# Kernel tuning notes

Hardware: AMD Instinct MI355X
Metric: run time of the kernel (lower is better)

## Reference

```python
import jax, jax.numpy as jnp
import numpy as np

B, C, H, W = 2, 4, 32, 256   # batch, num_classes (class 0 = background), range-image H x W
N = H * W                    # candidate points per (batch, class)
RADIUS = 3.0
KM_ITERS = 1
COORD_SCALE = 60.0           # spread lidar x/y so radius-3 NMS is non-trivial


def setup_inputs() -> dict:
    key = jax.random.key(0)
    k1, k2 = jax.random.split(key)
    segmented_channels = jax.random.normal(k1, (B, C, H, W), dtype=jnp.float32)
    lidar = jax.random.normal(k2, (B, 2, H, W), dtype=jnp.float32) * COORD_SCALE
    return {"segmented_channels": segmented_channels, "lidar": lidar}


def _radius_nms(points, mask, radius):
    # Greedy radius NMS in index order: keep point i iff no earlier kept point
    # lies within `radius`. Masked-out points are never kept (keep init = mask).
    n = points.shape[0]
    idx = jnp.arange(n)
    r2 = radius * radius

    def step(keep, i):
        d2 = jnp.sum((points - points[i]) ** 2, axis=-1)       # [N]
        suppress = keep & (d2 < r2) & (idx > i) & keep[i]
        return keep & ~suppress, None

    keep, _ = jax.lax.scan(step, mask, idx)
    return keep


def _kmeans(points, mask, keep, iters):
    # Centers initialized at the NMS-kept points (same index space as points).
    # Each valid class point is assigned to nearest valid center; centers move
    # to the mean of their assigned points.
    n = points.shape[0]
    centers = points
    w = mask.astype(points.dtype)
    BIG = jnp.asarray(1e30, points.dtype)
    for _ in range(iters):
        d2 = jnp.sum((points[:, None, :] - centers[None, :, :]) ** 2, axis=-1)  # [N,N]
        d2 = jnp.where(keep[None, :], d2, BIG)
        assign = jnp.argmin(d2, axis=1)                         # [N]
        sums = jax.ops.segment_sum(points * w[:, None], assign, num_segments=n)
        cnt = jax.ops.segment_sum(w, assign, num_segments=n)
        upd = sums / jnp.maximum(cnt, 1.0)[:, None]
        centers = jnp.where((keep & (cnt > 0))[:, None], upd, centers)
    return centers * keep[:, None].astype(points.dtype)


def reference(segmented_channels, lidar):
    ind = jnp.argmax(segmented_channels, axis=1)                # [B,H,W] class id per cell
    pts = jnp.stack([lidar[:, 0], lidar[:, 1]], axis=-1).reshape(B, N, 2)
    # boolean class masks for foreground classes 1..C-1
    cls_mask = jnp.stack([ind == c for c in range(1, C)], axis=1).reshape(B, C - 1, N)
    pts_all = jnp.broadcast_to(pts[:, None], (B, C - 1, N, 2)).reshape(B * (C - 1), N, 2)
    mask_all = cls_mask.reshape(B * (C - 1), N)

    def per_bc(args):
        p, m = args
        keep = _radius_nms(p, m, RADIUS)
        centers = _kmeans(p, m, keep, KM_ITERS)
        return centers, keep

    centers, keep = jax.lax.map(per_bc, (pts_all, mask_all))
    # centers: padded [B, C-1, N, 2]; keep marks which rows are real detections
    return centers.reshape(B, C - 1, N, 2), keep.reshape(B, C - 1, N)
```

## Files before the change

kernel.cpp:

```cpp
#include <hip/hip_runtime.h>

#define NPTS 8192
#define BCLS 4
#define NP   6
#define R2   9.0f
#define RAD  3.0f
#define GRD  128
#define NCELL (GRD*GRD)
#define PCAP 2048
#define CAP  4096
#define KBLK 64
#define KTHR 256
#define NSL  8
#define WBLK (NP*NSL)
#define WTHR 256

#define ST_U 0u
#define ST_A 1u
#define ST_D 2u


__global__ __launch_bounds__(KTHR) void k_front(
    const float* __restrict__ seg, const float* __restrict__ lidar,
    float* __restrict__ xs, float* __restrict__ ys,
    unsigned int* __restrict__ ns, unsigned int* __restrict__ counts,
    float* __restrict__ ksum, float* __restrict__ out)
{
    const int tid = threadIdx.x, lane = tid & 63;
    const int idx = blockIdx.x * KTHR + tid;
    const int b = idx >> 13, n = idx & 8191;

    __shared__ float ex[KTHR], ey[KTHR];
    __shared__ unsigned short en[KTHR];
    __shared__ unsigned int cnt6[6], off6[6], pos6[6];

    if (tid < 6) cnt6[tid] = 0;
    __syncthreads();

    const float* segb = seg + (size_t)b * BCLS * NPTS + n;
    float bv = segb[0];
    int bc = 0;
    #pragma unroll
    for (int c = 1; c < BCLS; ++c) {
        float v = segb[(size_t)c * NPTS];
        if (v > bv) { bv = v; bc = c; }
    }
    const float x = lidar[(size_t)b * 2 * NPTS + n];
    const float y = lidar[(size_t)b * 2 * NPTS + NPTS + n];
    const int p = (bc > 0) ? (b * 3 + bc - 1) : -1;

    #pragma unroll
    for (int q = 0; q < 6; ++q) {
        unsigned long long bal = __ballot(p == q);
        if (lane == 0 && bal) atomicAdd(&cnt6[q], (unsigned int)__popcll(bal));
    }
    __syncthreads();
    if (tid == 0) {
        unsigned int a = 0;
        #pragma unroll
        for (int q = 0; q < 6; ++q) { off6[q] = a; pos6[q] = a; a += cnt6[q]; }
    }
    __syncthreads();
    #pragma unroll
    for (int q = 0; q < 6; ++q) {
        unsigned long long bal = __ballot(p == q);
        if (bal) {
            int ldr = __builtin_ctzll(bal);
            unsigned int wb = 0;
            if (lane == ldr) wb = atomicAdd(&pos6[q], (unsigned int)__popcll(bal));
            wb = __shfl(wb, ldr, 64);
            if (p == q) {
                unsigned int s = wb + (unsigned int)__popcll(bal & ((1ull << lane) - 1ull));
                ex[s] = x; ey[s] = y; en[s] = (unsigned short)n;
            }
        }
    }
    __syncthreads();
    {
        const unsigned int total = off6[5] + cnt6[5];
        const int gbase = blockIdx.x * KTHR;
        for (int k = tid; k < (int)total; k += KTHR) {
            xs[gbase + k] = ex[k];
            ys[gbase + k] = ey[k];
            ns[gbase + k] = (unsigned int)en[k];
        }
        if (tid < 6) counts[blockIdx.x * 6 + tid] = cnt6[tid];
    }
    {
        float4* o4 = (float4*)out;
        for (int k = idx; k < 36864; k += KBLK * KTHR)
            o4[k] = make_float4(0.f, 0.f, 0.f, 0.f);
        float4* s4 = (float4*)ksum;
        for (int k = idx; k < 18432; k += KBLK * KTHR)
            s4[k] = make_float4(0.f, 0.f, 0.f, 0.f);
    }
}

__global__ __launch_bounds__(1024) void k_mid(
    const float* __restrict__ xs, const float* __restrict__ ys,
    const unsigned int* __restrict__ ns, const unsigned int* __restrict__ counts,
    float2* __restrict__ sps_g, unsigned int* __restrict__ cmb_g,
    unsigned int* __restrict__ cellpack_g, float* __restrict__ bbox_g,
    int* __restrict__ M_g,
    unsigned long long* __restrict__ ballots_g, unsigned int* __restrict__ base_g)
{
    const int p = blockIdx.x;
    const int tid = threadIdx.x, lane = tid & 63, wv = tid >> 6;

    __shared__ float2 sps[CAP];
    __shared__ unsigned int cmb[CAP];
    __shared__ unsigned int cellpack[NCELL];
    __shared__ unsigned short plist[2][PCAP];
    __shared__ int pcnt[2];
    __shared__ unsigned long long ballots[64];
    __shared__ unsigned int base64[64];
    __shared__ unsigned int wtot[16];
    __shared__ float redbuf[4][16];
    __shared__ unsigned int csrc[KBLK], cdst[KBLK];
    __shared__ float sbminx, sbminy, scell;
    __shared__ int sM;

    for (int k = tid; k < CAP; k += 1024) cmb[k] = ST_U;
    for (int k = tid; k < NCELL; k += 1024) cellpack[k] = 0u;
    if (tid == 0) { pcnt[0] = 0; pcnt[1] = 0; }

    if (wv == 0) {
        unsigned int c6[6];
        #pragma unroll
        for (int q = 0; q < 6; ++q) c6[q] = counts[lane * 6 + q];
        unsigned int within = 0;
        for (int q = 0; q < p; ++q) within += c6[q];
        unsigned int len = c6[p];
        unsigned int v = len;
        for (int d = 1; d < 64; d <<= 1) {
            unsigned int u = __shfl_up(v, d, 64);
            if (lane >= d) v += u;
        }
        csrc[lane] = lane * KTHR + within;
        cdst[lane] = v - len;
        if (lane == 63) sM = (int)(v < CAP ? v : CAP);
    }
    __syncthreads();
    const int M = sM;

    float xq[4], yq[4];
    unsigned int nq[4];
    int liq[4];
    {
        float mnx = 3e38f, mxx = -3e38f, mny = 3e38f, mxy = -3e38f;
        #pragma unroll
        for (int q = 0; q < 4; ++q) {
            int li = q * 1024 + tid;
            liq[q] = li;
            if (li < M) {
                int lo = 0, hi = KBLK - 1;
                #pragma unroll
                for (int s = 0; s < 6; ++s) {
                    int mid = (lo + hi + 1) >> 1;
                    if (cdst[mid] <= (unsigned int)li) lo = mid; else hi = mid - 1;
                }
                int si = csrc[lo] + (li - cdst[lo]);
                float x = xs[si], y = ys[si];
                xq[q] = x; yq[q] = y; nq[q] = ns[si];
                mnx = fminf(mnx, x); mxx = fmaxf(mxx, x);
                mny = fminf(mny, y); mxy = fmaxf(mxy, y);
            }
        }
        for (int d = 32; d; d >>= 1) {
            mnx = fminf(mnx, __shfl_xor(mnx, d, 64));
            mxx = fmaxf(mxx, __shfl_xor(mxx, d, 64));
            mny = fminf(mny, __shfl_xor(mny, d, 64));
            mxy = fmaxf(mxy, __shfl_xor(mxy, d, 64));
        }
        if (lane == 0) { redbuf[0][wv] = mnx; redbuf[1][wv] = mxx;
                         redbuf[2][wv] = mny; redbuf[3][wv] = mxy; }
    }
    __syncthreads();
    if (tid == 0) {
        float a = redbuf[0][0], b2 = redbuf[1][0], c = redbuf[2][0], d = redbuf[3][0];
        for (int q = 1; q < 16; ++q) {
            a = fminf(a, redbuf[0][q]); b2 = fmaxf(b2, redbuf[1][q]);
            c = fminf(c, redbuf[2][q]); d = fmaxf(d, redbuf[3][q]);
        }
        sbminx = a; sbminy = c;
        scell = fmaxf(2.0f * RAD, fmaxf(b2 - a, d - c) / 127.0f);
    }
    __syncthreads();
    const float bminx = sbminx, bminy = sbminy, inv = 1.0f / scell;

    int cellq[4];
    #pragma unroll
    for (int q = 0; q < 4; ++q) {
        if (liq[q] < M) {
            int ix = min(GRD - 1, max(0, (int)((xq[q] - bminx) * inv)));
            int iy = min(GRD - 1, max(0, (int)((yq[q] - bminy) * inv)));
            cellq[q] = iy * GRD + ix;
            atomicAdd(&cellpack[cellq[q]], 1u);
        } else cellq[q] = -1;
    }
    __syncthreads();
    {
        unsigned int c16[16], t16 = 0;
        #pragma unroll
        for (int q = 0; q < 16; ++q) { c16[q] = cellpack[tid * 16 + q]; t16 += c16[q]; }
        unsigned int v = t16;
        for (int d = 1; d < 64; d <<= 1) {
            unsigned int u = __shfl_up(v, d, 64);
            if (lane >= d) v += u;
        }
        if (lane == 63) wtot[wv] = v;
        __syncthreads();
        if (tid == 0) {
            unsigned int acc = 0;
            for (int q = 0; q < 16; ++q) { unsigned int t = wtot[q]; wtot[q] = acc; acc += t; }
        }
        __syncthreads();
        unsigned int excl = wtot[wv] + v - t16;
        #pragma unroll
        for (int q = 0; q < 16; ++q) { cellpack[tid * 16 + q] = excl << 16; excl += c16[q]; }
    }
    __syncthreads();
    #pragma unroll
    for (int q = 0; q < 4; ++q) {
        if (cellq[q] >= 0) {
            unsigned int old = atomicAdd(&cellpack[cellq[q]], 1u);
            unsigned int pos = (old >> 16) + (old & 0xffffu);
            sps[pos] = make_float2(xq[q], yq[q]);
            cmb[pos] = (nq[q] << 2) | ST_U;
        }
    }
    __syncthreads();

    const int pb = p * CAP;
    for (int k = tid; k < CAP; k += 1024) sps_g[pb + k] = sps[k];
    for (int k = tid; k < NCELL; k += 1024) cellpack_g[p * NCELL + k] = cellpack[k];
    if (tid == 0) {
        bbox_g[p * 4 + 0] = bminx; bbox_g[p * 4 + 1] = bminy;
        bbox_g[p * 4 + 2] = inv;
        M_g[p] = M;
    }

    #define ROW_FLAGS(CY, CX0, CX1, NI, ME, DEAD, UNDEC)                          \
    {                                                                             \
        unsigned int wa = cellpack[(CY) * GRD + (CX0)];                           \
        unsigned int wb = cellpack[(CY) * GRD + (CX1)];                           \
        unsigned int f0 = wa >> 16, f1 = (wb >> 16) + (wb & 0xffffu);             \
        for (unsigned int f = f0; f < f1; ++f) {                                  \
            unsigned int wf = cmb[f];                                             \
            float2 q = sps[f];                                                    \
            float dx = __fsub_rn((ME).x, q.x), dy = __fsub_rn((ME).y, q.y);       \
            float d2 = __fadd_rn(__fmul_rn(dx, dx), __fmul_rn(dy, dy));           \
            bool in = (d2 < R2) & ((int)(wf >> 2) < (NI));                        \
            DEAD  |= in & ((wf & 3u) == ST_A);                                    \
            UNDEC |= in & ((wf & 3u) == ST_U);                                    \
        }                                                                         \
    }
    #define SCAN_FLAGS(NI, ME, DEAD, UNDEC)                                       \
    {                                                                             \
        int cx0 = max(0, (int)(((ME).x - RAD - bminx) * inv));                    \
        int cx1 = min(GRD - 1, (int)(((ME).x + RAD - bminx) * inv));              \
        int cy0 = max(0, (int)(((ME).y - RAD - bminy) * inv));                    \
        int cy1 = min(GRD - 1, (int)(((ME).y + RAD - bminy) * inv));              \
        DEAD = false; UNDEC = false;                                              \
        ROW_FLAGS(cy0, cx0, cx1, NI, ME, DEAD, UNDEC);                            \
        if (cy1 > cy0) ROW_FLAGS(cy1, cx0, cx1, NI, ME, DEAD, UNDEC);             \
    }

    for (int e = tid; e < M; e += 1024) {
        unsigned int w = cmb[e];
        int ni = (int)(w >> 2);
        float2 me = sps[e];
        bool dead, undec;
        SCAN_FLAGS(ni, me, dead, undec);
        if (dead) cmb[e] = (w & ~3u) | ST_D;
        else if (!undec) cmb[e] = (w & ~3u) | ST_A;
        bool pendf = !dead && undec;
        unsigned long long act = __ballot(true);
        unsigned long long bal = __ballot(pendf);
        int leader = __builtin_ctzll(act);
        int cnt = __popcll(bal);
        int wbase = 0;
        if (lane == leader && cnt) wbase = atomicAdd(&pcnt[0], cnt);
        wbase = __shfl(wbase, leader, 64);
        if (pendf) {
            int pos = wbase + __popcll(bal & ((1ull << lane) - 1ull));
            if (pos < PCAP) plist[0][pos] = (unsigned short)e;
        }
    }

    int cur = 0;
    for (int round = 0; round < NPTS; ++round) {
        __syncthreads();
        int pc = pcnt[cur];
        if (pc == 0) break;
        if (pc > PCAP) {
            for (;;) {
                bool any = false;
                __syncthreads();
                for (int e = tid; e < M; e += 1024) {
                    unsigned int w = cmb[e];
                    if ((w & 3u) != ST_U) continue;
                    int ni = (int)(w >> 2);
                    float2 me = sps[e];
                    bool dead, undec;
                    SCAN_FLAGS(ni, me, dead, undec);
                    if (dead) cmb[e] = (w & ~3u) | ST_D;
                    else if (!undec) cmb[e] = (w & ~3u) | ST_A;
                    else any = true;
                }
                if (__syncthreads_count(any) == 0) break;
            }
            break;
        }
        if (tid == 0) pcnt[cur ^ 1] = 0;
        __syncthreads();
        for (int idx = tid; idx < pc; idx += 1024) {
            int e = plist[cur][idx];
            unsigned int w = cmb[e];
            int ni = (int)(w >> 2);
            float2 me = sps[e];
            bool dead, undec;
            SCAN_FLAGS(ni, me, dead, undec);
            if (dead) cmb[e] = (w & ~3u) | ST_D;
            else if (!undec) cmb[e] = (w & ~3u) | ST_A;
            bool pendf = !dead && undec;
            unsigned long long act = __ballot(true);
            unsigned long long bal = __ballot(pendf);
            int leader = __builtin_ctzll(act);
            int cnt = __popcll(bal);
            int wbase = 0;
            if (lane == leader && cnt) wbase = atomicAdd(&pcnt[cur ^ 1], cnt);
            wbase = __shfl(wbase, leader, 64);
            if (pendf) {
                int pos = wbase + __popcll(bal & ((1ull << lane) - 1ull));
                if (pos < PCAP) plist[cur ^ 1][pos] = (unsigned short)e;
            }
        }
        cur ^= 1;
    }
    __syncthreads();

    for (int k = 0; k < 4; ++k) {
        int e = (k << 10) + tid;
        unsigned long long bal = __ballot((cmb[e] & 3u) == ST_A);
        if (lane == 0) ballots[(k << 4) + wv] = bal;
    }
    __syncthreads();
    if (wv == 0) {
        unsigned int s = (unsigned int)__popcll(ballots[lane]);
        unsigned int v = s;
        for (int d = 1; d < 64; d <<= 1) {
            unsigned int u = __shfl_up(v, d, 64);
            if (lane >= d) v += u;
        }
        base64[lane] = v - s;
    }
    __syncthreads();
    for (int k = tid; k < CAP; k += 1024) cmb_g[pb + k] = cmb[k];
    if (tid < 64) { ballots_g[(p << 6) + tid] = ballots[tid]; base_g[(p << 6) + tid] = base64[tid]; }
}

#define KRANK_G(P, E) ((int)base_g[((P) << 6) + ((E) >> 6)] +                     \
    __popcll(ballots_g[((P) << 6) + ((E) >> 6)] & ((1ull << ((E) & 63)) - 1ull)))

__global__ __launch_bounds__(WTHR) void k_assign(
    const float2* __restrict__ sps_g, const unsigned int* __restrict__ cmb_g,
    const unsigned int* __restrict__ cellpack_g, const float* __restrict__ bbox_g,
    const int* __restrict__ M_g,
    const unsigned long long* __restrict__ ballots_g, const unsigned int* __restrict__ base_g,
    float* __restrict__ ksx, float* __restrict__ ksy, float* __restrict__ kcn)
{
    const int p = blockIdx.x / NSL, s = blockIdx.x % NSL;
    const int tid = threadIdx.x;
    const int M = M_g[p];
    const float bminx = bbox_g[p * 4], bminy = bbox_g[p * 4 + 1], inv = bbox_g[p * 4 + 2];
    const float2* sp = sps_g + p * CAP;
    const unsigned int* cm = cmb_g + p * CAP;
    const unsigned int* cp = cellpack_g + p * NCELL;

    const int chunk = (M + NSL - 1) / NSL;
    const int e0 = s * chunk, e1 = min(M, e0 + chunk);

    #define G_ROW_ARGMIN(CY, CX0, CX1, ME, BD, BE, BN)                            \
    {                                                                             \
        unsigned int wa = cp[(CY) * GRD + (CX0)];                                 \
        unsigned int wb = cp[(CY) * GRD + (CX1)];                                 \
        unsigned int f0 = wa >> 16, f1 = (wb >> 16) + (wb & 0xffffu);             \
        for (unsigned int f = f0; f < f1; ++f) {                                  \
            unsigned int wf = cm[f];                                              \
            float2 q = sp[f];                                                     \
            float dx = __fsub_rn((ME).x, q.x), dy = __fsub_rn((ME).y, q.y);       \
            float d2 = __fadd_rn(__fmul_rn(dx, dx), __fmul_rn(dy, dy));           \
            int nf = (int)(wf >> 2);                                              \
            bool better = ((wf & 3u) == ST_A) &                                   \
                          ((d2 < BD) | ((d2 == BD) & (nf < BN)));                 \
            BD = better ? d2 : BD;                                                \
            BE = better ? (int)f : BE;                                            \
            BN = better ? nf : BN;                                                \
        }                                                                         \
    }
    for (int e = e0 + tid; e < e1; e += WTHR) {
        unsigned int w = cm[e];
        float2 me = sp[e];
        int be;
        if ((w & 3u) == ST_A) {
            be = e;
        } else {
            int cx0 = max(0, (int)((me.x - RAD - bminx) * inv));
            int cx1 = min(GRD - 1, (int)((me.x + RAD - bminx) * inv));
            int cy0 = max(0, (int)((me.y - RAD - bminy) * inv));
            int cy1 = min(GRD - 1, (int)((me.y + RAD - bminy) * inv));
            float bd = 3e38f;
            be = -1;
            int bn = 1 << 30;
            G_ROW_ARGMIN(cy0, cx0, cx1, me, bd, be, bn);
            if (cy1 > cy0) G_ROW_ARGMIN(cy1, cx0, cx1, me, bd, be, bn);
            if (be < 0) continue;
        }
        int r = KRANK_G(p, be);
        atomicAdd(&ksx[p * CAP + r], me.x);
        atomicAdd(&ksy[p * CAP + r], me.y);
        atomicAdd(&kcn[p * CAP + r], 1.0f);
    }
}

__global__ __launch_bounds__(WTHR) void k_out(
    const unsigned int* __restrict__ cmb_g, const int* __restrict__ M_g,
    const unsigned long long* __restrict__ ballots_g, const unsigned int* __restrict__ base_g,
    const float* __restrict__ ksx, const float* __restrict__ ksy,
    const float* __restrict__ kcn, float* __restrict__ out)
{
    const int p = blockIdx.x / NSL, s = blockIdx.x % NSL;
    const int tid = threadIdx.x;
    const int M = M_g[p];
    const unsigned int* cm = cmb_g + p * CAP;
    const int base = p * NPTS;
    float* ok = out + (size_t)2 * NP * NPTS + base;

    const int chunk = (M + NSL - 1) / NSL;
    const int e0 = s * chunk, e1 = min(M, e0 + chunk);

    for (int e = e0 + tid; e < e1; e += WTHR) {
        unsigned int w = cm[e];
        if ((w & 3u) != ST_A) continue;
        int n = (int)(w >> 2);
        int r = KRANK_G(p, e);
        float c = kcn[p * CAP + r];
        out[2 * (base + n)]     = ksx[p * CAP + r] / c;
        out[2 * (base + n) + 1] = ksy[p * CAP + r] / c;
        ok[n] = 1.0f;
    }
}

extern "C" void kernel_launch(void* const* d_in, const int* in_sizes, int n_in,
                              void* d_out, int out_size, void* d_ws, size_t ws_size,
                              hipStream_t stream) {
    const float* seg   = (const float*)d_in[0];
    const float* lidar = (const float*)d_in[1];
    float* out = (float*)d_out;
    float* wsf = (float*)d_ws;

    float* xs = wsf;
    float* ys = wsf + 16384;
    unsigned int* ns = (unsigned int*)(wsf + 32768);
    unsigned int* counts = (unsigned int*)(wsf + 49152);
    float2* sps_g = (float2*)(wsf + 49536);
    unsigned int* cmb_g = (unsigned int*)(wsf + 98688);
    unsigned int* cellpack_g = (unsigned int*)(wsf + 123264);
    float* bbox_g = wsf + 221568;
    int* M_g = (int*)(wsf + 221592);
    unsigned long long* ballots_g = (unsigned long long*)(wsf + 221600);
    unsigned int* base_g = (unsigned int*)(wsf + 222368);
    float* ksx = wsf + 222752;
    float* ksy = wsf + 247328;
    float* kcn = wsf + 271904;

    k_front <<<KBLK, KTHR, 0, stream>>>(seg, lidar, xs, ys, ns, counts, ksx, out);
    k_mid   <<<NP, 1024, 0, stream>>>(xs, ys, ns, counts, sps_g, cmb_g, cellpack_g,
                                      bbox_g, M_g, ballots_g, base_g);
    k_assign<<<WBLK, WTHR, 0, stream>>>(sps_g, cmb_g, cellpack_g, bbox_g, M_g,
                                        ballots_g, base_g, ksx, ksy, kcn);
    k_out   <<<WBLK, WTHR, 0, stream>>>(cmb_g, M_g, ballots_g, base_g, ksx, ksy, kcn, out);
}
```

Before: 101.1 us.

## Replace iterative parallel NMS rounds with single-wave chunked sequential resolution

Replaces the block-wide fixed-point rounds of greedy radius NMS, which used pending lists and many __syncthreads, with a single wavefront. That wave processes points in original index order in 64-point chunks. Within each chunk, intra-chunk neighbor bitmasks are resolved with ballot loops, and already-decided earlier chunks are checked through the grid. An index-sorted list is built with bitmap scan to define the order. This removes the per-round barriers but serializes the work onto one wave out of 16, so per-chunk latency dominates.

Result: slower. 183.8 us (+81.7%).

```diff
diff --git a/kernel.cpp b/kernel.cpp
--- a/kernel.cpp
+++ b/kernel.cpp
@@ -7,7 +7,6 @@
 #define RAD  3.0f
 #define GRD  128
 #define NCELL (GRD*GRD)
-#define PCAP 2048
 #define CAP  4096
 #define KBLK 64
 #define KTHR 256
@@ -110,8 +109,11 @@
     __shared__ float2 sps[CAP];
     __shared__ unsigned int cmb[CAP];
     __shared__ unsigned int cellpack[NCELL];
-    __shared__ unsigned short plist[2][PCAP];
-    __shared__ int pcnt[2];
+    __shared__ unsigned short idxOf[NPTS];
+    __shared__ unsigned short slist[CAP];
+    __shared__ unsigned char chunkLane[CAP];
+    __shared__ unsigned long long pb[128];
+    __shared__ unsigned int woff[128];
     __shared__ unsigned long long ballots[64];
     __shared__ unsigned int base64[64];
     __shared__ unsigned int wtot[16];
@@ -122,7 +124,7 @@
 
     for (int k = tid; k < CAP; k += 1024) cmb[k] = ST_U;
     for (int k = tid; k < NCELL; k += 1024) cellpack[k] = 0u;
-    if (tid == 0) { pcnt[0] = 0; pcnt[1] = 0; }
+    if (tid < 128) pb[tid] = 0ull;
 
     if (wv == 0) {
         unsigned int c6[6];
@@ -231,16 +233,45 @@
     }
     __syncthreads();
 
-    const int pb = p * CAP;
-    for (int k = tid; k < CAP; k += 1024) sps_g[pb + k] = sps[k];
+    for (int e = tid; e < M; e += 1024) {
+        unsigned int n = cmb[e] >> 2;
+        idxOf[n] = (unsigned short)e;
+        atomicOr(&pb[n >> 6], 1ull << (n & 63));
+    }
+    const int pb_ = p * CAP;
+    for (int k = tid; k < CAP; k += 1024) sps_g[pb_ + k] = sps[k];
     for (int k = tid; k < NCELL; k += 1024) cellpack_g[p * NCELL + k] = cellpack[k];
     if (tid == 0) {
         bbox_g[p * 4 + 0] = bminx; bbox_g[p * 4 + 1] = bminy;
         bbox_g[p * 4 + 2] = inv;
         M_g[p] = M;
     }
-
-    #define ROW_FLAGS(CY, CX0, CX1, NI, ME, DEAD, UNDEC)                          \
+    __syncthreads();
+
+    if (wv == 0) {
+        unsigned int c0 = (unsigned int)__popcll(pb[2 * lane]);
+        unsigned int c1 = (unsigned int)__popcll(pb[2 * lane + 1]);
+        unsigned int s = c0 + c1, v = s;
+        for (int d = 1; d < 64; d <<= 1) {
+            unsigned int u = __shfl_up(v, d, 64);
+            if (lane >= d) v += u;
+        }
+        woff[2 * lane] = v - s;
+        woff[2 * lane + 1] = v - c1;
+    }
+    __syncthreads();
+    if (tid < 128) {
+        unsigned long long w = pb[tid];
+        unsigned int o = woff[tid];
+        while (w) {
+            int b = __builtin_ctzll(w);
+            w &= w - 1;
+            slist[o++] = idxOf[(tid << 6) + b];
+        }
+    }
+    __syncthreads();
+
+    #define SER_ROW(CY, CX0, CX1, NI, ME, EXTD, NBR)                              \
     {                                                                             \
         unsigned int wa = cellpack[(CY) * GRD + (CX0)];                           \
         unsigned int wb = cellpack[(CY) * GRD + (CX1)];                           \
@@ -251,92 +282,46 @@
             float dx = __fsub_rn((ME).x, q.x), dy = __fsub_rn((ME).y, q.y);       \
             float d2 = __fadd_rn(__fmul_rn(dx, dx), __fmul_rn(dy, dy));           \
             bool in = (d2 < R2) & ((int)(wf >> 2) < (NI));                        \
-            DEAD  |= in & ((wf & 3u) == ST_A);                                    \
-            UNDEC |= in & ((wf & 3u) == ST_U);                                    \
+            unsigned int st = wf & 3u;                                            \
+            EXTD |= in & (st == ST_A);                                            \
+            if (in & (st == ST_U)) NBR |= 1ull << chunkLane[f];                   \
         }                                                                         \
     }
-    #define SCAN_FLAGS(NI, ME, DEAD, UNDEC)                                       \
-    {                                                                             \
-        int cx0 = max(0, (int)(((ME).x - RAD - bminx) * inv));                    \
-        int cx1 = min(GRD - 1, (int)(((ME).x + RAD - bminx) * inv));              \
-        int cy0 = max(0, (int)(((ME).y - RAD - bminy) * inv));                    \
-        int cy1 = min(GRD - 1, (int)(((ME).y + RAD - bminy) * inv));              \
-        DEAD = false; UNDEC = false;                                              \
-        ROW_FLAGS(cy0, cx0, cx1, NI, ME, DEAD, UNDEC);                            \
-        if (cy1 > cy0) ROW_FLAGS(cy1, cx0, cx1, NI, ME, DEAD, UNDEC);             \
-    }
-
-    for (int e = tid; e < M; e += 1024) {
-        unsigned int w = cmb[e];
-        int ni = (int)(w >> 2);
-        float2 me = sps[e];
-        bool dead, undec;
-        SCAN_FLAGS(ni, me, dead, undec);
-        if (dead) cmb[e] = (w & ~3u) | ST_D;
-        else if (!undec) cmb[e] = (w & ~3u) | ST_A;
-        bool pendf = !dead && undec;
-        unsigned long long act = __ballot(true);
-        unsigned long long bal = __ballot(pendf);
-        int leader = __builtin_ctzll(act);
-        int cnt = __popcll(bal);
-        int wbase = 0;
-        if (lane == leader && cnt) wbase = atomicAdd(&pcnt[0], cnt);
-        wbase = __shfl(wbase, leader, 64);
-        if (pendf) {
-            int pos = wbase + __popcll(bal & ((1ull << lane) - 1ull));
-            if (pos < PCAP) plist[0][pos] = (unsigned short)e;
-        }
-    }
-
-    int cur = 0;
-    for (int round = 0; round < NPTS; ++round) {
-        __syncthreads();
-        int pc = pcnt[cur];
-        if (pc == 0) break;
-        if (pc > PCAP) {
-            for (;;) {
-                bool any = false;
-                __syncthreads();
-                for (int e = tid; e < M; e += 1024) {
-                    unsigned int w = cmb[e];
-                    if ((w & 3u) != ST_U) continue;
-                    int ni = (int)(w >> 2);
-                    float2 me = sps[e];
-                    bool dead, undec;
-                    SCAN_FLAGS(ni, me, dead, undec);
-                    if (dead) cmb[e] = (w & ~3u) | ST_D;
-                    else if (!undec) cmb[e] = (w & ~3u) | ST_A;
-                    else any = true;
-                }
-                if (__syncthreads_count(any) == 0) break;
-            }
-            break;
-        }
-        if (tid == 0) pcnt[cur ^ 1] = 0;
-        __syncthreads();
-        for (int idx = tid; idx < pc; idx += 1024) {
-            int e = plist[cur][idx];
+    if (wv == 0) {
+        const int nch = (M + 63) >> 6;
+        for (int c = 0; c < nch; ++c) {
+            int i = (c << 6) + lane;
+            bool act = i < M;
+            int e = act ? (int)slist[i] : 0;
             unsigned int w = cmb[e];
             int ni = (int)(w >> 2);
             float2 me = sps[e];
-            bool dead, undec;
-            SCAN_FLAGS(ni, me, dead, undec);
-            if (dead) cmb[e] = (w & ~3u) | ST_D;
-            else if (!undec) cmb[e] = (w & ~3u) | ST_A;
-            bool pendf = !dead && undec;
-            unsigned long long act = __ballot(true);
-            unsigned long long bal = __ballot(pendf);
-            int leader = __builtin_ctzll(act);
-            int cnt = __popcll(bal);
-            int wbase = 0;
-            if (lane == leader && cnt) wbase = atomicAdd(&pcnt[cur ^ 1], cnt);
-            wbase = __shfl(wbase, leader, 64);
-            if (pendf) {
-                int pos = wbase + __popcll(bal & ((1ull << lane) - 1ull));
-                if (pos < PCAP) plist[cur ^ 1][pos] = (unsigned short)e;
+            if (act) chunkLane[e] = (unsigned char)lane;
+            bool extdead = false;
+            unsigned long long nbr = 0ull;
+            if (act) {
+                int cx0 = max(0, (int)((me.x - RAD - bminx) * inv));
+                int cx1 = min(GRD - 1, (int)((me.x + RAD - bminx) * inv));
+                int cy0 = max(0, (int)((me.y - RAD - bminy) * inv));
+                int cy1 = min(GRD - 1, (int)((me.y + RAD - bminy) * inv));
+                SER_ROW(cy0, cx0, cx1, ni, me, extdead, nbr);
+                if (cy1 > cy0) SER_ROW(cy1, cx0, cx1, ni, me, extdead, nbr);
             }
-        }
-        cur ^= 1;
+            bool decided = !act, kept = false;
+            unsigned long long decidedM = __ballot(decided);
+            unsigned long long keptM = 0ull;
+            while (decidedM != ~0ull) {
+                bool dienow = !decided && (extdead || ((nbr & keptM) != 0ull));
+                bool keepnow = !decided && !dienow && ((nbr & ~decidedM) == 0ull);
+                unsigned long long dM = __ballot(dienow);
+                unsigned long long kM = __ballot(keepnow);
+                keptM |= kM;
+                decidedM |= dM | kM;
+                decided = decided || dienow || keepnow;
+                kept = kept || keepnow;
+            }
+            if (act) cmb[e] = (w & ~3u) | (kept ? ST_A : ST_D);
+        }
     }
     __syncthreads();
 
@@ -356,7 +341,7 @@
         base64[lane] = v - s;
     }
     __syncthreads();
-    for (int k = tid; k < CAP; k += 1024) cmb_g[pb + k] = cmb[k];
+    for (int k = tid; k < CAP; k += 1024) cmb_g[pb_ + k] = cmb[k];
     if (tid < 64) { ballots_g[(p << 6) + tid] = ballots[tid]; base_g[(p << 6) + tid] = base64[tid]; }
 }
 
```
